# Kernel tuning notes

Measured on AMD Instinct MI355X. Metric: run time of the kernel, lower is better.

Reference implementation:

```python
import jax, jax.numpy as jnp
import numpy as np

N, D_IN, D_C, D_Q, K = 4096, 64, 32, 128, 3


def setup_inputs() -> dict:
    key = jax.random.key(0)
    ks = jax.random.split(key, 16)
    rn = lambda k, shp, s: jax.random.normal(k, shp, dtype=jnp.float32) * s
    inp = {
        "x": rn(ks[0], (N, D_IN), 1.0),
        "comms": rn(ks[1], (N, D_C), 0.1),
        # dense positive transition matrix (all entries nonzero -> the
        # trans==0 -> -inf masking step is a faithful no-op here)
        "trans": jax.random.uniform(ks[2], (N, N), dtype=jnp.float32, minval=0.01, maxval=1.0),
        "mask": jnp.ones((N,), dtype=jnp.int32),
        # encoding: Linear(num_inputs + comm_channels, ch_q)
        "W_enc": rn(ks[3], (D_IN + D_C, D_Q), 1.0 / np.sqrt(D_IN + D_C)),
        "b_enc": rn(ks[4], (D_Q,), 0.01),
        # att_decoding[k]: Linear(ch_q, ch_q)
        "W_ad": rn(ks[5], (K, D_Q, D_Q), 1.0 / np.sqrt(D_Q)),
        "b_ad": rn(ks[6], (K, D_Q), 0.01),
        # att[k]: Linear(2*ch_q, 1)
        "w_att": rn(ks[7], (K, 2 * D_Q), 1.0 / np.sqrt(2 * D_Q)),
        "b_att": rn(ks[8], (K,), 0.01),
        # att_vectors[k]: Linear(ch_q, ch_q)
        "W_av": rn(ks[9], (K, D_Q, D_Q), 1.0 / np.sqrt(D_Q)),
        "b_av": rn(ks[10], (K, D_Q), 0.01),
        # decoding: Linear(ch_q, 1)
        "W_dec": rn(ks[11], (D_Q,), 1.0 / np.sqrt(D_Q)),
        "b_dec": rn(ks[12], (), 0.01),
    }
    return inp


def reference(x, comms, trans, mask, W_enc, b_enc, W_ad, b_ad, w_att, b_att,
              W_av, b_av, W_dec, b_dec):
    dq = W_ad.shape[-1]
    # encoding of [node features, communication vector]
    h = jnp.concatenate([x, comms], axis=-1) @ W_enc + b_enc          # (n, dq)
    # trans.transpose(0,1); zeros -> -inf (additive log-mask)
    tb = trans.T
    tb = jnp.where(tb == 0, -jnp.inf, tb)                              # (n, n)
    for k in range(K):
        att = h @ W_ad[k] + b_ad[k]                                    # (n, dq)
        # concat-GAT score: score[i,j] = w_a . att[j] + w_b . att[i] + b
        # (decomposition of Linear(cat(att_t, att_t^T)) -> avoids n x n x 2dq)
        wa, wb = w_att[k, :dq], w_att[k, dq:]
        score = (att @ wb)[:, None] + (att @ wa)[None, :] + b_att[k]   # (n, n)
        focus = jax.nn.softmax(score + tb, axis=1)                     # (n, n)
        v = h @ W_av[k] + b_av[k]                                      # (n, dq)
        h = focus @ v                                                  # (n, dq)
    out = h @ W_dec + b_dec                                            # (n,)
    # final masking (args.rl = False branch): masked nodes -> -inf
    s = out + jnp.where(mask == 0, -jnp.inf, 0.0).astype(out.dtype)
    return s
```

## Files before the change

kernel.cpp:

```cpp
#include <hip/hip_runtime.h>
#include <math.h>

#define N 4096
#define DQ 128
#define DIN 64
#define DC 32
#define NT 9
#define PST9 144
#define PST1 16
#define NIT 256

typedef __attribute__((ext_vector_type(8))) short short8;
typedef __attribute__((ext_vector_type(8))) _Float16 half8;
typedef __attribute__((ext_vector_type(4))) float f32x4;

__device__ __forceinline__ unsigned short f2h(float x) {
  return __builtin_bit_cast(unsigned short, (_Float16)x);
}
__device__ __forceinline__ void async16(unsigned short* lds, const unsigned short* g) {
  __builtin_amdgcn_global_load_lds(
      (const __attribute__((address_space(1))) void*)g,
      (__attribute__((address_space(3))) void*)lds, 16, 0, 0);
}

__global__ __launch_bounds__(256) void kExp(const float* __restrict__ trans,
                                            unsigned short* __restrict__ Ef) {
  __shared__ float sh[32 * 65];
  const int tid = threadIdx.x;
  const int ig = blockIdx.x;
  const int kt = blockIdx.y;
  const int r = tid >> 3;
  const int c8 = (tid & 7) * 8;
  const float* src = &trans[((size_t)kt * 32 + r) * N + ig * 64 + c8];
  const float4 v0 = *(const float4*)src;
  const float4 v1 = *(const float4*)(src + 4);
  float* d = &sh[r * 65 + c8];
  d[0] = __expf(v0.x); d[1] = __expf(v0.y); d[2] = __expf(v0.z); d[3] = __expf(v0.w);
  d[4] = __expf(v1.x); d[5] = __expf(v1.y); d[6] = __expf(v1.z); d[7] = __expf(v1.w);
  __syncthreads();
  const int itl = tid >> 6;
  const int lane = tid & 63;
  const int quad = lane >> 4, l15 = lane & 15;
  const int col = itl * 16 + l15;
  unsigned short hb[8];
#pragma unroll
  for (int jj = 0; jj < 8; ++jj) hb[jj] = f2h(sh[(quad * 8 + jj) * 65 + col]);
  const short8 s = {(short)hb[0], (short)hb[1], (short)hb[2], (short)hb[3],
                    (short)hb[4], (short)hb[5], (short)hb[6], (short)hb[7]};
  *(short8*)(Ef + (((size_t)kt * NIT + ig * 4 + itl) * 64 + lane) * 8) = s;
}

__device__ __forceinline__ void v_phase(const float* hs_row, float p,
    const float* __restrict__ W_av_k, const float* __restrict__ b_av_k,
    int r, int d4, unsigned short* shh) {
  float a[4] = {b_av_k[d4], b_av_k[d4 + 1], b_av_k[d4 + 2], b_av_k[d4 + 3]};
  for (int c = 0; c < DQ; ++c) {
    const float hv = hs_row[c];
    const float4 w = *(const float4*)&W_av_k[c * DQ + d4];
    a[0] += hv * w.x; a[1] += hv * w.y; a[2] += hv * w.z; a[3] += hv * w.w;
  }
  const int nt = d4 >> 4;
#pragma unroll
  for (int e = 0; e < 4; ++e)
    shh[nt * 128 + ((d4 + e) & 15) * 8 + r] = f2h(p * a[e]);
  const int c32 = d4 >> 2;
  if (c32 < 16)
    shh[8 * 128 + c32 * 8 + r] = (c32 == 0) ? f2h(p) : 0;
}

__device__ __forceinline__ void v_store(int tid, int blk,
    const unsigned short* shh, unsigned short* __restrict__ Vf) {
  const int kt = blk >> 2, quad = blk & 3;
  if (tid < NT * 16) {
    const int nt = tid >> 4, l15 = tid & 15;
    const size_t dst = (((size_t)kt * NT + nt) * 64 + quad * 16 + l15) * 8;
    *(short8*)(Vf + dst) = *(const short8*)&shh[nt * 128 + l15 * 8];
  }
}

__global__ __launch_bounds__(256) void kVS0(const float* __restrict__ x,
    const float* __restrict__ comms, const float* __restrict__ W_enc,
    const float* __restrict__ b_enc, const float* __restrict__ W_ad_k,
    const float* __restrict__ wa, const float* __restrict__ W_av_k,
    const float* __restrict__ b_av_k, unsigned short* __restrict__ Vf) {
  __shared__ float xs[8][96];
  __shared__ float hs[8][DQ];
  __shared__ float u[DQ];
  __shared__ float pb[8];
  __shared__ __align__(16) unsigned short shh[NT * 128];
  const int tid = threadIdx.x;
  const int blk = blockIdx.x;
  if (tid < 128) {
    const float4 v = *(const float4*)&x[(size_t)blk * 8 * DIN + tid * 4];
    const int idx = tid * 4, r = idx >> 6, c = idx & 63;
    xs[r][c] = v.x; xs[r][c + 1] = v.y; xs[r][c + 2] = v.z; xs[r][c + 3] = v.w;
  } else if (tid < 192) {
    const int t = tid - 128;
    const float4 v = *(const float4*)&comms[(size_t)blk * 8 * DC + t * 4];
    const int idx = t * 4, r = idx >> 5, c = idx & 31;
    xs[r][64 + c] = v.x; xs[r][64 + c + 1] = v.y; xs[r][64 + c + 2] = v.z; xs[r][64 + c + 3] = v.w;
  }
  if (tid < DQ) {
    float s = 0.f;
    const float* wrow = &W_ad_k[tid * DQ];
    for (int q = 0; q < DQ; ++q) s += wrow[q] * wa[q];
    u[tid] = s;
  }
  __syncthreads();
  const int r = tid >> 5;
  const int c32 = tid & 31;
  const int d4 = c32 * 4;
  {
    float a0 = b_enc[d4], a1 = b_enc[d4 + 1], a2 = b_enc[d4 + 2], a3 = b_enc[d4 + 3];
    for (int c = 0; c < 96; ++c) {
      const float hv = xs[r][c];
      const float4 w = *(const float4*)&W_enc[c * DQ + d4];
      a0 += hv * w.x; a1 += hv * w.y; a2 += hv * w.z; a3 += hv * w.w;
    }
    hs[r][d4] = a0; hs[r][d4 + 1] = a1; hs[r][d4 + 2] = a2; hs[r][d4 + 3] = a3;
  }
  __syncthreads();
  float part = 0.f;
  for (int c = c32; c < DQ; c += 32) part += hs[r][c] * u[c];
#pragma unroll
  for (int m = 16; m > 0; m >>= 1) part += __shfl_xor(part, m, 32);
  if (c32 == 0) pb[r] = __expf(part);
  __syncthreads();
  v_phase(hs[r], pb[r], W_av_k, b_av_k, r, d4, shh);
  __syncthreads();
  v_store(tid, blk, shh, Vf);
}

__global__ __launch_bounds__(256) void kVSR(const float* __restrict__ P,
    const float* __restrict__ W_ad_k, const float* __restrict__ wa,
    const float* __restrict__ W_av_k, const float* __restrict__ b_av_k,
    unsigned short* __restrict__ Vf, int ksplit) {
  __shared__ float hs[8][DQ];
  __shared__ float u[DQ];
  __shared__ float pb[8];
  __shared__ __align__(16) unsigned short shh[NT * 128];
  const int tid = threadIdx.x;
  const int r = tid >> 5;
  const int c32 = tid & 31;
  const int d4 = c32 * 4;
  const int j = blockIdx.x * 8 + r;
  if (tid < DQ) {
    float s = 0.f;
    const float* wrow = &W_ad_k[tid * DQ];
    for (int q = 0; q < DQ; ++q) s += wrow[q] * wa[q];
    u[tid] = s;
  }
  float4 num = {0.f, 0.f, 0.f, 0.f};
  float den = 0.f;
  for (int s = 0; s < ksplit; ++s) {
    const float* b = &P[((size_t)s * N + j) * PST9];
    const float4 v = *(const float4*)&b[d4];
    num.x += v.x; num.y += v.y; num.z += v.z; num.w += v.w;
    den += b[128];
  }
  const float inv = 1.f / den;
  hs[r][d4] = num.x * inv; hs[r][d4 + 1] = num.y * inv;
  hs[r][d4 + 2] = num.z * inv; hs[r][d4 + 3] = num.w * inv;
  __syncthreads();
  float part = 0.f;
  for (int c = c32; c < DQ; c += 32) part += hs[r][c] * u[c];
#pragma unroll
  for (int m = 16; m > 0; m >>= 1) part += __shfl_xor(part, m, 32);
  if (c32 == 0) pb[r] = __expf(part);
  __syncthreads();
  v_phase(hs[r], pb[r], W_av_k, b_av_k, r, d4, shh);
  __syncthreads();
  v_store(tid, blockIdx.x, shh, Vf);
}

__global__ __launch_bounds__(256) void kVSRc(const float* __restrict__ P,
    const float* __restrict__ W_ad_k, const float* __restrict__ wa,
    const float* __restrict__ W_av_k, const float* __restrict__ b_av_k,
    const float* __restrict__ W_dec, unsigned short* __restrict__ Vc,
    int ksplit) {
  __shared__ float hs[8][DQ];
  __shared__ float u[DQ];
  __shared__ float pb[8];
  const int tid = threadIdx.x;
  const int r = tid >> 5;
  const int c32 = tid & 31;
  const int d4 = c32 * 4;
  const int j = blockIdx.x * 8 + r;
  if (tid < DQ) {
    float s = 0.f;
    const float* wrow = &W_ad_k[tid * DQ];
    for (int q = 0; q < DQ; ++q) s += wrow[q] * wa[q];
    u[tid] = s;
  }
  float4 num = {0.f, 0.f, 0.f, 0.f};
  float den = 0.f;
  for (int s = 0; s < ksplit; ++s) {
    const float* b = &P[((size_t)s * N + j) * PST9];
    const float4 v = *(const float4*)&b[d4];
    num.x += v.x; num.y += v.y; num.z += v.z; num.w += v.w;
    den += b[128];
  }
  const float inv = 1.f / den;
  hs[r][d4] = num.x * inv; hs[r][d4 + 1] = num.y * inv;
  hs[r][d4 + 2] = num.z * inv; hs[r][d4 + 3] = num.w * inv;
  __syncthreads();
  float part = 0.f;
  for (int c = c32; c < DQ; c += 32) part += hs[r][c] * u[c];
#pragma unroll
  for (int m = 16; m > 0; m >>= 1) part += __shfl_xor(part, m, 32);
  if (c32 == 0) pb[r] = __expf(part);
  __syncthreads();
  float a[4] = {b_av_k[d4], b_av_k[d4 + 1], b_av_k[d4 + 2], b_av_k[d4 + 3]};
  for (int c = 0; c < DQ; ++c) {
    const float hv = hs[r][c];
    const float4 w = *(const float4*)&W_av_k[c * DQ + d4];
    a[0] += hv * w.x; a[1] += hv * w.y; a[2] += hv * w.z; a[3] += hv * w.w;
  }
  float vd = a[0] * W_dec[d4] + a[1] * W_dec[d4 + 1]
           + a[2] * W_dec[d4 + 2] + a[3] * W_dec[d4 + 3];
#pragma unroll
  for (int m = 16; m > 0; m >>= 1) vd += __shfl_xor(vd, m, 32);
  const float p = pb[r];
  if (c32 < 16) {
    const int blk = blockIdx.x;
    const size_t ix = (((size_t)(blk >> 2)) * 64 + (blk & 3) * 16 + c32) * 8 + r;
    Vc[ix] = (c32 == 0) ? f2h(p * vd) : (c32 == 1) ? f2h(p) : 0;
  }
}

template <int NTT, int PST>
__global__ __launch_bounds__(256) void kGemm(
    const unsigned short* __restrict__ Ef, const unsigned short* __restrict__ Vf,
    float* __restrict__ P, int nsteps) {
  __shared__ __align__(16) unsigned short lds[8 * NTT * 512];
  const int tid = threadIdx.x;
  const int w = tid >> 6, lane = tid & 63;
  const int quad = lane >> 4, l15 = lane & 15;
  const int it0 = blockIdx.x * 8 + w * 2;

  f32x4 acc[2][NTT];
#pragma unroll
  for (int ti = 0; ti < 2; ++ti)
#pragma unroll
    for (int nt = 0; nt < NTT; ++nt) acc[ti][nt] = (f32x4){0.f, 0.f, 0.f, 0.f};

  for (int ss = 0; ss < nsteps; ss += 8) {
    const size_t kt0 = (size_t)blockIdx.y * nsteps + ss;
    if (ss) __syncthreads();
    for (int c = w; c < 8 * NTT; c += 4)
      async16(&lds[c * 512], Vf + (kt0 * NTT + c) * 512 + lane * 8);
    half8 A[2][8];
#pragma unroll
    for (int ti = 0; ti < 2; ++ti)
#pragma unroll
      for (int s = 0; s < 8; ++s)
        A[ti][s] = __builtin_bit_cast(half8,
            *(const short8*)(Ef + (((kt0 + s) * NIT + it0 + ti) * 64 + lane) * 8));
    __syncthreads();
#pragma unroll
    for (int s = 0; s < 8; ++s) {
#pragma unroll
      for (int nt = 0; nt < NTT; ++nt) {
        const half8 Bh = __builtin_bit_cast(half8,
            *(const short8*)(lds + (s * NTT + nt) * 512 + lane * 8));
        acc[0][nt] = __builtin_amdgcn_mfma_f32_16x16x32_f16(A[0][s], Bh, acc[0][nt], 0, 0, 0);
        acc[1][nt] = __builtin_amdgcn_mfma_f32_16x16x32_f16(A[1][s], Bh, acc[1][nt], 0, 0, 0);
      }
    }
  }
  float* Pb = P + (size_t)blockIdx.y * N * PST;
#pragma unroll
  for (int ti = 0; ti < 2; ++ti) {
#pragma unroll
    for (int nt = 0; nt < NTT; ++nt) {
#pragma unroll
      for (int r = 0; r < 4; ++r) {
        const int i = (it0 + ti) * 16 + quad * 4 + r;
        Pb[(size_t)i * PST + nt * 16 + l15] = acc[ti][nt][r];
      }
    }
  }
}

__global__ __launch_bounds__(256) void kOut(const float* __restrict__ P3,
    const float* __restrict__ b_dec, const int* __restrict__ mask,
    float* __restrict__ out, int ksplit) {
  const int i = blockIdx.x * 256 + threadIdx.x;
  float num = 0.f, den = 0.f;
  for (int s = 0; s < ksplit; ++s) {
    const float* b = &P3[((size_t)s * N + i) * PST1];
    num += b[0];
    den += b[1];
  }
  out[i] = (mask[i] == 0) ? -INFINITY : num / den + b_dec[0];
}

extern "C" void kernel_launch(void* const* d_in, const int* in_sizes, int n_in,
                              void* d_out, int out_size, void* d_ws, size_t ws_size,
                              hipStream_t stream) {
  (void)in_sizes; (void)n_in; (void)out_size;
  const float* x     = (const float*)d_in[0];
  const float* comms = (const float*)d_in[1];
  const float* trans = (const float*)d_in[2];
  const int*   mask  = (const int*)d_in[3];
  const float* W_enc = (const float*)d_in[4];
  const float* b_enc = (const float*)d_in[5];
  const float* W_ad  = (const float*)d_in[6];
  const float* w_att = (const float*)d_in[8];
  const float* W_av  = (const float*)d_in[10];
  const float* b_av  = (const float*)d_in[11];
  const float* W_dec = (const float*)d_in[12];
  const float* b_dec = (const float*)d_in[13];
  float* out         = (float*)d_out;

  char* ws = (char*)d_ws;
  unsigned short* Vf = (unsigned short*)ws;  ws += (size_t)(N / 32) * NT * 512 * 2;
  unsigned short* Vc = (unsigned short*)ws;  ws += (size_t)(N / 32) * 512 * 2;
  unsigned short* Ef = (unsigned short*)ws;  ws += (size_t)N * N * 2;
  float* P  = (float*)ws;
  const size_t fixedB = (size_t)(N / 32) * (NT + 1) * 1024 + (size_t)N * N * 2;
  const size_t perB   = (size_t)N * (PST9 + PST1) * 4;
  const int ksplit = (ws_size >= fixedB + 16 * perB) ? 16 : 8;
  float* P3 = P + (size_t)ksplit * N * PST9;
  const int nsteps = (N / ksplit) >> 5;

  kExp<<<dim3(64, 128), 256, 0, stream>>>(trans, Ef);
  kVS0<<<N / 8, 256, 0, stream>>>(x, comms, W_enc, b_enc, W_ad, w_att,
                                  W_av, b_av, Vf);
  kGemm<NT, PST9><<<dim3(NIT / 8, ksplit), 256, 0, stream>>>(Ef, Vf, P, nsteps);

  kVSR<<<N / 8, 256, 0, stream>>>(P, W_ad + (size_t)1 * DQ * DQ,
                                  w_att + 2 * DQ, W_av + (size_t)1 * DQ * DQ,
                                  b_av + DQ, Vf, ksplit);
  kGemm<NT, PST9><<<dim3(NIT / 8, ksplit), 256, 0, stream>>>(Ef, Vf, P, nsteps);

  kVSRc<<<N / 8, 256, 0, stream>>>(P, W_ad + (size_t)2 * DQ * DQ,
                                   w_att + 4 * DQ, W_av + (size_t)2 * DQ * DQ,
                                   b_av + 2 * DQ, W_dec, Vc, ksplit);
  kGemm<1, PST1><<<dim3(NIT / 8, ksplit), 256, 0, stream>>>(Ef, Vc, P3, nsteps);

  kOut<<<N / 256, 256, 0, stream>>>(P3, b_dec, mask, out, ksplit);
}
```

Before: 229.5 us.

## Restructure GEMM to per-wave K-split with double-buffered async loads and LDS reduction

The GEMM now gives each wave its own K-slice over a pair of row tiles, in place of splitting row tiles across waves. Each wave streams its slice with double-buffered async LDS loads and register prefetch of the E tiles, synchronised by waitcnt rather than block-wide barriers. The four wave partials are then reduced in LDS before storing. The global K-split is fixed at 4, which shrinks the partial buffer and the reduction work in the downstream kernels. Grid size becomes 128x4 blocks, trading fewer global partials for more blocks and extra LDS reduction traffic.

```diff
diff --git a/kernel.cpp b/kernel.cpp
--- a/kernel.cpp
+++ b/kernel.cpp
@@ -9,6 +9,8 @@
 #define PST9 144
 #define PST1 16
 #define NIT 256
+#define KB 4
+#define SW 8
 
 typedef __attribute__((ext_vector_type(8))) short short8;
 typedef __attribute__((ext_vector_type(8))) _Float16 half8;
@@ -134,7 +136,7 @@
 __global__ __launch_bounds__(256) void kVSR(const float* __restrict__ P,
     const float* __restrict__ W_ad_k, const float* __restrict__ wa,
     const float* __restrict__ W_av_k, const float* __restrict__ b_av_k,
-    unsigned short* __restrict__ Vf, int ksplit) {
+    unsigned short* __restrict__ Vf) {
   __shared__ float hs[8][DQ];
   __shared__ float u[DQ];
   __shared__ float pb[8];
@@ -152,7 +154,8 @@
   }
   float4 num = {0.f, 0.f, 0.f, 0.f};
   float den = 0.f;
-  for (int s = 0; s < ksplit; ++s) {
+#pragma unroll
+  for (int s = 0; s < KB; ++s) {
     const float* b = &P[((size_t)s * N + j) * PST9];
     const float4 v = *(const float4*)&b[d4];
     num.x += v.x; num.y += v.y; num.z += v.z; num.w += v.w;
@@ -176,8 +179,7 @@
 __global__ __launch_bounds__(256) void kVSRc(const float* __restrict__ P,
     const float* __restrict__ W_ad_k, const float* __restrict__ wa,
     const float* __restrict__ W_av_k, const float* __restrict__ b_av_k,
-    const float* __restrict__ W_dec, unsigned short* __restrict__ Vc,
-    int ksplit) {
+    const float* __restrict__ W_dec, unsigned short* __restrict__ Vc) {
   __shared__ float hs[8][DQ];
   __shared__ float u[DQ];
   __shared__ float pb[8];
@@ -194,7 +196,8 @@
   }
   float4 num = {0.f, 0.f, 0.f, 0.f};
   float den = 0.f;
-  for (int s = 0; s < ksplit; ++s) {
+#pragma unroll
+  for (int s = 0; s < KB; ++s) {
     const float* b = &P[((size_t)s * N + j) * PST9];
     const float4 v = *(const float4*)&b[d4];
     num.x += v.x; num.y += v.y; num.z += v.z; num.w += v.w;
@@ -229,14 +232,16 @@
 }
 
 template <int NTT, int PST>
-__global__ __launch_bounds__(256) void kGemm(
+__global__ __launch_bounds__(256) void kGemmR(
     const unsigned short* __restrict__ Ef, const unsigned short* __restrict__ Vf,
-    float* __restrict__ P, int nsteps) {
-  __shared__ __align__(16) unsigned short lds[8 * NTT * 512];
+    float* __restrict__ P) {
+  __shared__ __align__(16) unsigned short lds[4 * 2 * NTT * 512];
   const int tid = threadIdx.x;
   const int w = tid >> 6, lane = tid & 63;
   const int quad = lane >> 4, l15 = lane & 15;
-  const int it0 = blockIdx.x * 8 + w * 2;
+  const int it0 = blockIdx.x * 2;
+  const size_t ktw = (size_t)blockIdx.y * (4 * SW) + w * SW;
+  unsigned short* myL = lds + w * (2 * NTT * 512);
 
   f32x4 acc[2][NTT];
 #pragma unroll
@@ -244,39 +249,67 @@
 #pragma unroll
     for (int nt = 0; nt < NTT; ++nt) acc[ti][nt] = (f32x4){0.f, 0.f, 0.f, 0.f};
 
-  for (int ss = 0; ss < nsteps; ss += 8) {
-    const size_t kt0 = (size_t)blockIdx.y * nsteps + ss;
-    if (ss) __syncthreads();
-    for (int c = w; c < 8 * NTT; c += 4)
-      async16(&lds[c * 512], Vf + (kt0 * NTT + c) * 512 + lane * 8);
-    half8 A[2][8];
-#pragma unroll
-    for (int ti = 0; ti < 2; ++ti)
-#pragma unroll
-      for (int s = 0; s < 8; ++s)
-        A[ti][s] = __builtin_bit_cast(half8,
-            *(const short8*)(Ef + (((kt0 + s) * NIT + it0 + ti) * 64 + lane) * 8));
-    __syncthreads();
-#pragma unroll
-    for (int s = 0; s < 8; ++s) {
-#pragma unroll
-      for (int nt = 0; nt < NTT; ++nt) {
-        const half8 Bh = __builtin_bit_cast(half8,
-            *(const short8*)(lds + (s * NTT + nt) * 512 + lane * 8));
-        acc[0][nt] = __builtin_amdgcn_mfma_f32_16x16x32_f16(A[0][s], Bh, acc[0][nt], 0, 0, 0);
-        acc[1][nt] = __builtin_amdgcn_mfma_f32_16x16x32_f16(A[1][s], Bh, acc[1][nt], 0, 0, 0);
-      }
-    }
-  }
+#pragma unroll
+  for (int c = 0; c < NTT; ++c)
+    async16(myL + c * 512, Vf + (ktw * NTT + c) * 512 + lane * 8);
+  half8 A0[2], A1[2];
+#pragma unroll
+  for (int ti = 0; ti < 2; ++ti)
+    A0[ti] = __builtin_bit_cast(half8,
+        *(const short8*)(Ef + ((ktw * NIT + it0 + ti) * 64 + lane) * 8));
+
+#pragma unroll
+  for (int t = 0; t < SW; ++t) {
+    if (t + 1 < SW) {
+      const size_t ktn = ktw + t + 1;
+#pragma unroll
+      for (int c = 0; c < NTT; ++c)
+        async16(myL + ((t + 1) & 1) * NTT * 512 + c * 512,
+                Vf + (ktn * NTT + c) * 512 + lane * 8);
+#pragma unroll
+      for (int ti = 0; ti < 2; ++ti)
+        A1[ti] = __builtin_bit_cast(half8,
+            *(const short8*)(Ef + ((ktn * NIT + it0 + ti) * 64 + lane) * 8));
+      __builtin_amdgcn_s_waitcnt(0xF70 | (NTT + 2));
+    } else {
+      __builtin_amdgcn_s_waitcnt(0xF70);
+    }
+    const unsigned short* bb = myL + (t & 1) * NTT * 512;
+#pragma unroll
+    for (int nt = 0; nt < NTT; ++nt) {
+      const half8 Bh = __builtin_bit_cast(half8,
+          *(const short8*)(bb + nt * 512 + lane * 8));
+      acc[0][nt] = __builtin_amdgcn_mfma_f32_16x16x32_f16(A0[0], Bh, acc[0][nt], 0, 0, 0);
+      acc[1][nt] = __builtin_amdgcn_mfma_f32_16x16x32_f16(A0[1], Bh, acc[1][nt], 0, 0, 0);
+    }
+    if (t + 1 < SW) { A0[0] = A1[0]; A0[1] = A1[1]; }
+  }
+  __syncthreads();
+  float* lf = (float*)lds;
+#pragma unroll
+  for (int ti = 0; ti < 2; ++ti)
+#pragma unroll
+    for (int nt = 0; nt < NTT; ++nt) {
+      float4 v; v.x = acc[ti][nt][0]; v.y = acc[ti][nt][1];
+      v.z = acc[ti][nt][2]; v.w = acc[ti][nt][3];
+      *(float4*)&lf[(w * 2 * NTT + ti * NTT + nt) * 256 + lane * 4] = v;
+    }
+  __syncthreads();
   float* Pb = P + (size_t)blockIdx.y * N * PST;
-#pragma unroll
-  for (int ti = 0; ti < 2; ++ti) {
-#pragma unroll
-    for (int nt = 0; nt < NTT; ++nt) {
+  for (int p = w; p < 2 * NTT; p += 4) {
+    const int ti = p / NTT, nt = p % NTT;
+    float4 s = {0.f, 0.f, 0.f, 0.f};
+#pragma unroll
+    for (int wv = 0; wv < 4; ++wv) {
+      const float4 v = *(const float4*)&lf[(wv * 2 * NTT + p) * 256 + lane * 4];
+      s.x += v.x; s.y += v.y; s.z += v.z; s.w += v.w;
+    }
+    const float sr[4] = {s.x, s.y, s.z, s.w};
+    if (NTT == 1 || nt != 8 || l15 == 0) {
 #pragma unroll
       for (int r = 0; r < 4; ++r) {
         const int i = (it0 + ti) * 16 + quad * 4 + r;
-        Pb[(size_t)i * PST + nt * 16 + l15] = acc[ti][nt][r];
+        Pb[(size_t)i * PST + nt * 16 + l15] = sr[r];
       }
     }
   }
@@ -284,10 +317,11 @@
 
 __global__ __launch_bounds__(256) void kOut(const float* __restrict__ P3,
     const float* __restrict__ b_dec, const int* __restrict__ mask,
-    float* __restrict__ out, int ksplit) {
+    float* __restrict__ out) {
   const int i = blockIdx.x * 256 + threadIdx.x;
   float num = 0.f, den = 0.f;
-  for (int s = 0; s < ksplit; ++s) {
+#pragma unroll
+  for (int s = 0; s < KB; ++s) {
     const float* b = &P3[((size_t)s * N + i) * PST1];
     num += b[0];
     den += b[1];
@@ -298,7 +332,7 @@
 extern "C" void kernel_launch(void* const* d_in, const int* in_sizes, int n_in,
                               void* d_out, int out_size, void* d_ws, size_t ws_size,
                               hipStream_t stream) {
-  (void)in_sizes; (void)n_in; (void)out_size;
+  (void)in_sizes; (void)n_in; (void)out_size; (void)ws_size;
   const float* x     = (const float*)d_in[0];
   const float* comms = (const float*)d_in[1];
   const float* trans = (const float*)d_in[2];
@@ -317,27 +351,23 @@
   unsigned short* Vf = (unsigned short*)ws;  ws += (size_t)(N / 32) * NT * 512 * 2;
   unsigned short* Vc = (unsigned short*)ws;  ws += (size_t)(N / 32) * 512 * 2;
   unsigned short* Ef = (unsigned short*)ws;  ws += (size_t)N * N * 2;
-  float* P  = (float*)ws;
-  const size_t fixedB = (size_t)(N / 32) * (NT + 1) * 1024 + (size_t)N * N * 2;
-  const size_t perB   = (size_t)N * (PST9 + PST1) * 4;
-  const int ksplit = (ws_size >= fixedB + 16 * perB) ? 16 : 8;
-  float* P3 = P + (size_t)ksplit * N * PST9;
-  const int nsteps = (N / ksplit) >> 5;
+  float* P  = (float*)ws;                    ws += (size_t)KB * N * PST9 * 4;
+  float* P3 = (float*)ws;
 
   kExp<<<dim3(64, 128), 256, 0, stream>>>(trans, Ef);
   kVS0<<<N / 8, 256, 0, stream>>>(x, comms, W_enc, b_enc, W_ad, w_att,
                                   W_av, b_av, Vf);
-  kGemm<NT, PST9><<<dim3(NIT / 8, ksplit), 256, 0, stream>>>(Ef, Vf, P, nsteps);
+  kGemmR<NT, PST9><<<dim3(NIT / 2, KB), 256, 0, stream>>>(Ef, Vf, P);
 
   kVSR<<<N / 8, 256, 0, stream>>>(P, W_ad + (size_t)1 * DQ * DQ,
                                   w_att + 2 * DQ, W_av + (size_t)1 * DQ * DQ,
-                                  b_av + DQ, Vf, ksplit);
-  kGemm<NT, PST9><<<dim3(NIT / 8, ksplit), 256, 0, stream>>>(Ef, Vf, P, nsteps);
+                                  b_av + DQ, Vf);
+  kGemmR<NT, PST9><<<dim3(NIT / 2, KB), 256, 0, stream>>>(Ef, Vf, P);
 
   kVSRc<<<N / 8, 256, 0, stream>>>(P, W_ad + (size_t)2 * DQ * DQ,
                                    w_att + 4 * DQ, W_av + (size_t)2 * DQ * DQ,
-                                   b_av + 2 * DQ, W_dec, Vc, ksplit);
-  kGemm<1, PST1><<<dim3(NIT / 8, ksplit), 256, 0, stream>>>(Ef, Vc, P3, nsteps);
-
-  kOut<<<N / 256, 256, 0, stream>>>(P3, b_dec, mask, out, ksplit);
-}
+                                   b_av + 2 * DQ, W_dec, Vc);
+  kGemmR<1, PST1><<<dim3(NIT / 2, KB), 256, 0, stream>>>(Ef, Vc, P3);
+
+  kOut<<<N / 256, 256, 0, stream>>>(P3, b_dec, mask, out);
+}
```

Measured after the change: 213.2 us. 7.1% less time.
